# Kernel optimization log

Measured on AMD Instinct MI355X. Metric: run time of the kernel, lower is better.

Reference implementation:

```python
import jax, jax.numpy as jnp
import numpy as np

N_NODES = 100000
N_EDGES = 800000
IN_DIM = 128
NUM_HEADS = 8
HEAD_DIM = 16  # out_dim // num_heads = 128 // 8


def setup_inputs() -> dict:
    key = jax.random.key(0)
    ks = jax.random.split(key, 10)
    scale = 1.0 / np.sqrt(IN_DIM)
    return {
        "x": jax.random.normal(ks[0], (N_NODES, IN_DIM), dtype=jnp.float32),
        "edge_index": jax.random.randint(ks[1], (2, N_EDGES), 0, N_NODES, dtype=jnp.int64),
        "virt_h": jax.random.normal(ks[2], (1, IN_DIM), dtype=jnp.float32),
        "virt_edge_index": jax.random.randint(ks[3], (2, 1), 0, 1, dtype=jnp.int64),
        "Wq": jax.random.normal(ks[4], (IN_DIM, NUM_HEADS * HEAD_DIM), dtype=jnp.float32) * scale,
        "bq": jnp.zeros((NUM_HEADS * HEAD_DIM,), dtype=jnp.float32),
        "Wk": jax.random.normal(ks[5], (IN_DIM, NUM_HEADS * HEAD_DIM), dtype=jnp.float32) * scale,
        "bk": jnp.zeros((NUM_HEADS * HEAD_DIM,), dtype=jnp.float32),
        "Wv": jax.random.normal(ks[6], (IN_DIM, NUM_HEADS * HEAD_DIM), dtype=jnp.float32) * scale,
        "bv": jnp.zeros((NUM_HEADS * HEAD_DIM,), dtype=jnp.float32),
    }


def reference(x, edge_index, virt_h, virt_edge_index, Wq, bq, Wk, bk, Wv, bv):
    # use_virt_nodes=False: virt_h / virt_edge_index are unused dummies.
    n = x.shape[0]
    H, D = NUM_HEADS, HEAD_DIM
    Q = (x @ Wq + bq).reshape(n, H, D)
    K = (x @ Wk + bk).reshape(n, H, D)
    V = (x @ Wv + bv).reshape(n, H, D)

    src = edge_index[0]
    dst = edge_index[1]

    # edge-wise gather QK dot -> clamp -> exp; score: [E, H, 1]
    dot = jnp.sum(K[src] * Q[dst], axis=-1, keepdims=True) / np.sqrt(D).astype(np.float32)
    score = jnp.exp(jnp.clip(dot, -5.0, 5.0))

    msg = V[src] * score  # [E, H, D]
    wV = jax.ops.segment_sum(msg, dst, num_segments=n)     # [N, H, D]
    Z = jax.ops.segment_sum(score, dst, num_segments=n)    # [N, H, 1]

    h_out = (wV / (Z + 1e-6)).reshape(n, H * D)
    return h_out
```

## Files before the change

### kernel.cpp

```cpp
#include <hip/hip_runtime.h>

#define IN_DIM   128
#define NH       8
#define HD       16
#define OUTD     128
#define QKVD     384
#define SH       7
#define NSORTB   64

typedef unsigned short ushort_t;
typedef unsigned int   uint_t;
typedef __bf16 bf16x8 __attribute__((ext_vector_type(8)));
typedef float  f32x4  __attribute__((ext_vector_type(4)));

__device__ __forceinline__ float bf2f(ushort_t u) {
    return __uint_as_float(((uint_t)u) << 16);
}
__device__ __forceinline__ ushort_t f2bf(float f) {
    uint_t u = __float_as_uint(f);
    u += 0x7FFFu + ((u >> 16) & 1u);
    return (ushort_t)(u >> 16);
}

__global__ __launch_bounds__(256) void prep_w(
    const float* __restrict__ Wq, const float* __restrict__ Wk,
    const float* __restrict__ Wv, ushort_t* __restrict__ Wt)
{
    __shared__ float ld[32][33];
    int mat  = blockIdx.x >> 4;
    int tile = blockIdx.x & 15;
    int k0 = (tile >> 2) * 32, c0 = (tile & 3) * 32;
    const float* W = (mat == 0) ? Wq : (mat == 1) ? Wk : Wv;
    int t = threadIdx.x;
    {
        int k = t >> 3, c4 = (t & 7) * 4;
        float4 f = *(const float4*)&W[(size_t)(k0 + k) * 128 + c0 + c4];
        ld[k][c4 + 0] = f.x; ld[k][c4 + 1] = f.y;
        ld[k][c4 + 2] = f.z; ld[k][c4 + 3] = f.w;
    }
    __syncthreads();
    {
        int c = t >> 3, kg = (t & 7) * 4;
        union { ushort_t h[4]; uint2 u; } o;
        o.h[0] = f2bf(ld[kg + 0][c]); o.h[1] = f2bf(ld[kg + 1][c]);
        o.h[2] = f2bf(ld[kg + 2][c]); o.h[3] = f2bf(ld[kg + 3][c]);
        *(uint2*)&Wt[((size_t)(mat * 128 + c0 + c)) * 128 + k0 + kg] = o.u;
    }
}

__global__ __launch_bounds__(384, 3) void fat_gemm_sort(
    const float* __restrict__ x, const ushort_t* __restrict__ Wt,
    const float* __restrict__ bq, const float* __restrict__ bk,
    const float* __restrict__ bv, ushort_t* __restrict__ qkv,
    const int* __restrict__ ei, int* __restrict__ aux,
    uint_t* __restrict__ regions,
    int N, int E, int ntiles, int NBC, int CH)
{
    __shared__ __align__(16) char smem[58448];

    if (blockIdx.x < NSORTB) {
        uint_t* recs = (uint_t*)smem;
        int* hist    = (int*)(smem + 50000);
        int* scn     = (int*)(smem + 54096);
        const int tid = threadIdx.x;
        const int blk = blockIdx.x;
        const int e0g = blk * CH;
        const int e1g = min(E, e0g + CH);
        const int m   = e1g - e0g;

        for (int i = tid; i < 1024; i += 384) hist[i] = 0;
        __syncthreads();
        for (int e = e0g + tid; e < e1g; e += 384)
            atomicAdd(&hist[ei[E + e] >> SH], 1);
        __syncthreads();
        if (tid < 64) {
            int base16 = tid * 16;
            int loc[16]; int s = 0;
#pragma unroll
            for (int i = 0; i < 16; i++) { loc[i] = s; s += hist[base16 + i]; }
            int incl = s;
            for (int off = 1; off < 64; off <<= 1) {
                int t = __shfl_up(incl, off);
                if (tid >= off) incl += t;
            }
            int cexcl = incl - s;
#pragma unroll
            for (int i = 0; i < 16; i++) scn[base16 + i] = cexcl + loc[i];
        }
        __syncthreads();
        for (int b = tid; b < NBC; b += 384) aux[b * NSORTB + blk] = scn[b];
        if (tid == 0) aux[NBC * NSORTB + blk] = m;
        __syncthreads();
        for (int e = e0g + tid; e < e1g; e += 384) {
            int d = ei[E + e];
            int src = ei[e];
            int slot = atomicAdd(&scn[d >> SH], 1);
            recs[slot] = (uint_t)src | ((uint_t)(d & 127) << 20);
        }
        __syncthreads();
        for (int s = tid; s < m; s += 384)
            regions[(size_t)blk * CH + s] = recs[s];
        return;
    }

    ushort_t* sh = (ushort_t*)smem;

    const int tid  = threadIdx.x;
    const int w    = tid >> 6;
    const int quad = (tid >> 4) & 3;
    const int l15  = tid & 15;
    const int colg = w << 6;

    bf16x8 bfr[4][4];
#pragma unroll
    for (int kt = 0; kt < 4; kt++)
#pragma unroll
        for (int cs = 0; cs < 4; cs++) {
            int col = colg + cs * 16 + l15;
            bfr[kt][cs] = *(const bf16x8*)&Wt[(size_t)col * 128 + kt * 32 + quad * 8];
        }

    const int mat = w >> 1;
    const float* Bp = (mat == 0) ? bq : (mat == 1) ? bk : bv;
    float bias[4];
#pragma unroll
    for (int cs = 0; cs < 4; cs++)
        bias[cs] = Bp[((w & 1) << 6) + cs * 16 + l15];

    const int gstride = (int)gridDim.x - NSORTB;
    for (int tile = (int)blockIdx.x - NSORTB; tile < ntiles; tile += gstride) {
        const int row0 = tile * 64;
        __syncthreads();

        for (int ch = tid; ch < 1024; ch += 384) {
            int row = ch >> 4;
            int kc  = ch & 15;
            int grow = row0 + row; if (grow > N - 1) grow = N - 1;
            const float* xp = x + (size_t)grow * IN_DIM + kc * 8;
            float4 f0 = *(const float4*)xp;
            float4 f1 = *(const float4*)(xp + 4);
            union { ushort_t h[8]; uint4 u; } tt;
            tt.h[0] = f2bf(f0.x); tt.h[1] = f2bf(f0.y);
            tt.h[2] = f2bf(f0.z); tt.h[3] = f2bf(f0.w);
            tt.h[4] = f2bf(f1.x); tt.h[5] = f2bf(f1.y);
            tt.h[6] = f2bf(f1.z); tt.h[7] = f2bf(f1.w);
            *(uint4*)&sh[(kc * 65 + row) * 8] = tt.u;
        }
        __syncthreads();

        f32x4 acc[4][4];
#pragma unroll
        for (int r = 0; r < 4; r++)
#pragma unroll
            for (int cs = 0; cs < 4; cs++) acc[r][cs] = (f32x4){0.f, 0.f, 0.f, 0.f};

#pragma unroll
        for (int kt = 0; kt < 4; kt++) {
            int kc = kt * 4 + quad;
            bf16x8 af[4];
#pragma unroll
            for (int r = 0; r < 4; r++)
                af[r] = *(const bf16x8*)&sh[(kc * 65 + r * 16 + l15) * 8];
#pragma unroll
            for (int r = 0; r < 4; r++)
#pragma unroll
                for (int cs = 0; cs < 4; cs++)
                    acc[r][cs] = __builtin_amdgcn_mfma_f32_16x16x32_bf16(
                        af[r], bfr[kt][cs], acc[r][cs], 0, 0, 0);
        }

#define EPS 392
#pragma unroll
        for (int qq = 0; qq < 4; qq++) {
            __syncthreads();
            int lrow = quad << 2;
#pragma unroll
            for (int cs = 0; cs < 4; cs++) {
                int col = (w << 6) + cs * 16 + l15;
#pragma unroll
                for (int reg = 0; reg < 4; reg++)
                    sh[(lrow + reg) * EPS + col] = f2bf(acc[qq][cs][reg] + bias[cs]);
            }
            __syncthreads();
#pragma unroll
            for (int i = 0; i < 2; i++) {
                int c = tid + i * 384;
                int row = c / 48;
                int col = (c % 48) * 8;
                int grow = row0 + qq * 16 + row;
                if (grow < N) {
                    uint4 val = *(const uint4*)&sh[row * EPS + col];
                    *(uint4*)&qkv[(size_t)grow * QKVD + col] = val;
                }
            }
        }
#undef EPS
    }
}

__global__ __launch_bounds__(256) void efine(
    const uint_t* __restrict__ regions, const int* __restrict__ aux,
    int* __restrict__ P, int* __restrict__ sorted_src,
    int N, int NBC, int CH)
{
    __shared__ int rl[64], ro[64], doff[64];
    __shared__ int cnt[128], scn2[128];
    __shared__ uint_t stage[4096];
    __shared__ int    sst[4096];
    __shared__ int s_base;
    const int tid = threadIdx.x;
    const int b   = blockIdx.x;

    if (tid < 64) {
        int r0 = aux[b * NSORTB + tid];
        int r1 = aux[(b + 1) * NSORTB + tid];
        ro[tid] = r0;
        rl[tid] = r1 - r0;
        doff[tid] = r1 - r0;
        int bsum = r0;
#pragma unroll
        for (int off = 1; off < 64; off <<= 1)
            bsum += __shfl_xor(bsum, off);
        if (tid == 0) s_base = bsum;
    }
    __syncthreads();
    for (int off = 1; off < 64; off <<= 1) {
        int v = (tid >= off && tid < 64) ? doff[tid - off] : 0;
        __syncthreads();
        if (tid < 64) doff[tid] += v;
        __syncthreads();
    }
    const int m = doff[63];
    const int base = s_base;

    {
        int r = tid >> 2, k = tid & 3;
        int dst0 = doff[r] - rl[r];
        int src0 = ro[r];
        int len  = rl[r];
        for (int i = k; i < len; i += 4)
            stage[dst0 + i] = regions[(size_t)r * CH + src0 + i];
    }
    __syncthreads();

    if (tid < 128) cnt[tid] = 0;
    __syncthreads();
    for (int i = tid; i < m; i += 256)
        atomicAdd(&cnt[stage[i] >> 20], 1);
    __syncthreads();
    if (tid < 128) scn2[tid] = cnt[tid];
    __syncthreads();
    for (int off = 1; off < 128; off <<= 1) {
        int v = (tid >= off && tid < 128) ? scn2[tid - off] : 0;
        __syncthreads();
        if (tid < 128) scn2[tid] += v;
        __syncthreads();
    }
    if (tid < 128) {
        int excl = scn2[tid] - cnt[tid];
        int n = b * 128 + tid;
        if (n < N) P[n] = base + excl;
        cnt[tid] = excl;
    }
    __syncthreads();
    for (int i = tid; i < m; i += 256) {
        uint_t r = stage[i];
        int pos = atomicAdd(&cnt[r >> 20], 1);
        sst[pos] = (int)(r & 0xFFFFFu);
    }
    __syncthreads();
    for (int i = tid; i < m; i += 256)
        sorted_src[base + i] = sst[i];
}

__global__ __launch_bounds__(256) void segment_attn(
    const ushort_t* __restrict__ qkv,
    const int* __restrict__ P, const int* __restrict__ sorted_src,
    float* __restrict__ out, int N, int E)
{
    int n = (blockIdx.x * 256 + threadIdx.x) >> 4;
    int g = threadIdx.x & 15;
    if (n >= N) return;
    int start = P[n];
    int end   = (n + 1 < N) ? P[n + 1] : E;
    int deg   = end - start;

    const uint_t* qrow = (const uint_t*)(qkv + (size_t)n * QKVD);
    uint4 qu = *(const uint4*)(qrow + g * 4);
    float q0 = bf2f((ushort_t)(qu.x & 0xFFFF)), q1 = bf2f((ushort_t)(qu.x >> 16));
    float q2 = bf2f((ushort_t)(qu.y & 0xFFFF)), q3 = bf2f((ushort_t)(qu.y >> 16));
    float q4 = bf2f((ushort_t)(qu.z & 0xFFFF)), q5 = bf2f((ushort_t)(qu.z >> 16));
    float q6 = bf2f((ushort_t)(qu.w & 0xFFFF)), q7 = bf2f((ushort_t)(qu.w >> 16));

    float a0 = 0.f, a1 = 0.f, a2 = 0.f, a3 = 0.f;
    float a4 = 0.f, a5 = 0.f, a6 = 0.f, a7 = 0.f, z = 0.f;

    int myidx = (g < deg) ? sorted_src[start + g] : 0;
    int wbase = (threadIdx.x & 63) & 48;

#define PROC(ku, vu)                                                       \
    {                                                                      \
        float p = bf2f((ushort_t)((ku).x & 0xFFFF)) * q0                   \
                + bf2f((ushort_t)((ku).x >> 16))    * q1                   \
                + bf2f((ushort_t)((ku).y & 0xFFFF)) * q2                   \
                + bf2f((ushort_t)((ku).y >> 16))    * q3                   \
                + bf2f((ushort_t)((ku).z & 0xFFFF)) * q4                   \
                + bf2f((ushort_t)((ku).z >> 16))    * q5                   \
                + bf2f((ushort_t)((ku).w & 0xFFFF)) * q6                   \
                + bf2f((ushort_t)((ku).w >> 16))    * q7;                  \
        p += __shfl_xor(p, 1);                                             \
        p = fminf(fmaxf(p * 0.25f, -5.f), 5.f);                            \
        float s = __expf(p);                                               \
        a0 += bf2f((ushort_t)((vu).x & 0xFFFF)) * s;                       \
        a1 += bf2f((ushort_t)((vu).x >> 16))    * s;                       \
        a2 += bf2f((ushort_t)((vu).y & 0xFFFF)) * s;                       \
        a3 += bf2f((ushort_t)((vu).y >> 16))    * s;                       \
        a4 += bf2f((ushort_t)((vu).z & 0xFFFF)) * s;                       \
        a5 += bf2f((ushort_t)((vu).z >> 16))    * s;                       \
        a6 += bf2f((ushort_t)((vu).w & 0xFFFF)) * s;                       \
        a7 += bf2f((ushort_t)((vu).w >> 16))    * s;                       \
        z += s;                                                            \
    }

    int cnt = (deg < 16) ? deg : 16;
    int t = 0;
    for (; t + 4 <= cnt; t += 4) {
        int s0 = __shfl(myidx, wbase + t);
        int s1 = __shfl(myidx, wbase + t + 1);
        int s2 = __shfl(myidx, wbase + t + 2);
        int s3 = __shfl(myidx, wbase + t + 3);
        const uint_t* kv0 = (const uint_t*)(qkv + (size_t)s0 * QKVD + 128);
        const uint_t* kv1 = (const uint_t*)(qkv + (size_t)s1 * QKVD + 128);
        const uint_t* kv2 = (const uint_t*)(qkv + (size_t)s2 * QKVD + 128);
        const uint_t* kv3 = (const uint_t*)(qkv + (size_t)s3 * QKVD + 128);
        uint4 ku0 = *(const uint4*)(kv0 + g * 4);
        uint4 ku1 = *(const uint4*)(kv1 + g * 4);
        uint4 ku2 = *(const uint4*)(kv2 + g * 4);
        uint4 ku3 = *(const uint4*)(kv3 + g * 4);
        uint4 vu0 = *(const uint4*)(kv0 + 64 + g * 4);
        uint4 vu1 = *(const uint4*)(kv1 + 64 + g * 4);
        uint4 vu2 = *(const uint4*)(kv2 + 64 + g * 4);
        uint4 vu3 = *(const uint4*)(kv3 + 64 + g * 4);
        PROC(ku0, vu0); PROC(ku1, vu1); PROC(ku2, vu2); PROC(ku3, vu3);
    }
    for (; t + 2 <= cnt; t += 2) {
        int s0 = __shfl(myidx, wbase + t);
        int s1 = __shfl(myidx, wbase + t + 1);
        const uint_t* kv0 = (const uint_t*)(qkv + (size_t)s0 * QKVD + 128);
        const uint_t* kv1 = (const uint_t*)(qkv + (size_t)s1 * QKVD + 128);
        uint4 ku0 = *(const uint4*)(kv0 + g * 4);
        uint4 ku1 = *(const uint4*)(kv1 + g * 4);
        uint4 vu0 = *(const uint4*)(kv0 + 64 + g * 4);
        uint4 vu1 = *(const uint4*)(kv1 + 64 + g * 4);
        PROC(ku0, vu0); PROC(ku1, vu1);
    }
    if (t < cnt) {
        int s0 = __shfl(myidx, wbase + t);
        const uint_t* kv0 = (const uint_t*)(qkv + (size_t)s0 * QKVD + 128);
        uint4 ku0 = *(const uint4*)(kv0 + g * 4);
        uint4 vu0 = *(const uint4*)(kv0 + 64 + g * 4);
        PROC(ku0, vu0);
    }
    for (int j = start + 16; j + 2 <= end; j += 2) {
        int s0 = sorted_src[j];
        int s1 = sorted_src[j + 1];
        const uint_t* kv0 = (const uint_t*)(qkv + (size_t)s0 * QKVD + 128);
        const uint_t* kv1 = (const uint_t*)(qkv + (size_t)s1 * QKVD + 128);
        uint4 ku0 = *(const uint4*)(kv0 + g * 4);
        uint4 ku1 = *(const uint4*)(kv1 + g * 4);
        uint4 vu0 = *(const uint4*)(kv0 + 64 + g * 4);
        uint4 vu1 = *(const uint4*)(kv1 + 64 + g * 4);
        PROC(ku0, vu0); PROC(ku1, vu1);
    }
    if (deg > 16 && ((deg - 16) & 1)) {
        int s0 = sorted_src[end - 1];
        const uint_t* kv0 = (const uint_t*)(qkv + (size_t)s0 * QKVD + 128);
        uint4 ku0 = *(const uint4*)(kv0 + g * 4);
        uint4 vu0 = *(const uint4*)(kv0 + 64 + g * 4);
        PROC(ku0, vu0);
    }
#undef PROC

    float inv = 1.f / (z + 1e-6f);
    f32x4 o0 = {a0 * inv, a1 * inv, a2 * inv, a3 * inv};
    f32x4 o1 = {a4 * inv, a5 * inv, a6 * inv, a7 * inv};
    float* ob = out + (size_t)n * OUTD + g * 8;
    __builtin_nontemporal_store(o0, (f32x4*)ob);
    __builtin_nontemporal_store(o1, (f32x4*)(ob + 4));
}

extern "C" void kernel_launch(void* const* d_in, const int* in_sizes, int n_in,
                              void* d_out, int out_size, void* d_ws, size_t ws_size,
                              hipStream_t stream) {
    const float* x  = (const float*)d_in[0];
    const int*   ei = (const int*)d_in[1];
    const float* Wq = (const float*)d_in[4];
    const float* bq = (const float*)d_in[5];
    const float* Wk = (const float*)d_in[6];
    const float* bk = (const float*)d_in[7];
    const float* Wv = (const float*)d_in[8];
    const float* bv = (const float*)d_in[9];
    float* out = (float*)d_out;

    const int N = in_sizes[0] / IN_DIM;
    const int E = in_sizes[1] / 2;
    const int NBC = (N + 127) >> 7;
    const int CH  = (E + NSORTB - 1) / NSORTB;

    char* wsb = (char*)d_ws;
    ushort_t* qkv = (ushort_t*)wsb;
    ushort_t* Wt  = qkv + (size_t)N * QKVD;
    int* aux = (int*)(Wt + 384 * 128);
    uint_t* regions = (uint_t*)(aux + (NBC + 1) * NSORTB);
    int* sorted = (int*)(regions + (size_t)NSORTB * CH);
    int* P = sorted + E;

    const int ntiles = (N + 63) / 64;

    prep_w<<<48, 256, 0, stream>>>(Wq, Wk, Wv, Wt);
    fat_gemm_sort<<<512, 384, 0, stream>>>(
        x, Wt, bq, bk, bv, qkv, ei, aux, regions, N, E, ntiles, NBC, CH);
    efine<<<NBC, 256, 0, stream>>>(regions, aux, P, sorted, N, NBC, CH);
    segment_attn<<<((size_t)N * 16 + 255) / 256, 256, 0, stream>>>(
        qkv, P, sorted, out, N, E);
}
```

Before: 243.5 us.

## Fuse weight prep, GEMM, sort and attention into one persistent megakernel

```diff
diff --git a/kernel.cpp b/kernel.cpp
--- a/kernel.cpp
+++ b/kernel.cpp
@@ -7,11 +7,14 @@
 #define QKVD     384
 #define SH       7
 #define NSORTB   64
+#define GRID     512
 
 typedef unsigned short ushort_t;
 typedef unsigned int   uint_t;
 typedef __bf16 bf16x8 __attribute__((ext_vector_type(8)));
 typedef float  f32x4  __attribute__((ext_vector_type(4)));
+
+#define AGT __HIP_MEMORY_SCOPE_AGENT
 
 __device__ __forceinline__ float bf2f(ushort_t u) {
     return __uint_as_float(((uint_t)u) << 16);
@@ -21,48 +24,30 @@
     u += 0x7FFFu + ((u >> 16) & 1u);
     return (ushort_t)(u >> 16);
 }
-
-__global__ __launch_bounds__(256) void prep_w(
-    const float* __restrict__ Wq, const float* __restrict__ Wk,
-    const float* __restrict__ Wv, ushort_t* __restrict__ Wt)
-{
-    __shared__ float ld[32][33];
-    int mat  = blockIdx.x >> 4;
-    int tile = blockIdx.x & 15;
-    int k0 = (tile >> 2) * 32, c0 = (tile & 3) * 32;
-    const float* W = (mat == 0) ? Wq : (mat == 1) ? Wk : Wv;
-    int t = threadIdx.x;
-    {
-        int k = t >> 3, c4 = (t & 7) * 4;
-        float4 f = *(const float4*)&W[(size_t)(k0 + k) * 128 + c0 + c4];
-        ld[k][c4 + 0] = f.x; ld[k][c4 + 1] = f.y;
-        ld[k][c4 + 2] = f.z; ld[k][c4 + 3] = f.w;
-    }
-    __syncthreads();
-    {
-        int c = t >> 3, kg = (t & 7) * 4;
-        union { ushort_t h[4]; uint2 u; } o;
-        o.h[0] = f2bf(ld[kg + 0][c]); o.h[1] = f2bf(ld[kg + 1][c]);
-        o.h[2] = f2bf(ld[kg + 2][c]); o.h[3] = f2bf(ld[kg + 3][c]);
-        *(uint2*)&Wt[((size_t)(mat * 128 + c0 + c)) * 128 + k0 + kg] = o.u;
-    }
+__device__ __forceinline__ void wait_ge(int* p, int target) {
+    while (__hip_atomic_load(p, __ATOMIC_RELAXED, AGT) < target)
+        __builtin_amdgcn_s_sleep(8);
 }
 
-__global__ __launch_bounds__(384, 3) void fat_gemm_sort(
-    const float* __restrict__ x, const ushort_t* __restrict__ Wt,
-    const float* __restrict__ bq, const float* __restrict__ bk,
-    const float* __restrict__ bv, ushort_t* __restrict__ qkv,
-    const int* __restrict__ ei, int* __restrict__ aux,
-    uint_t* __restrict__ regions,
-    int N, int E, int ntiles, int NBC, int CH)
+__global__ __launch_bounds__(384, 3) void mega(
+    const float* __restrict__ x,
+    const float* __restrict__ Wq, const float* __restrict__ bq,
+    const float* __restrict__ Wk, const float* __restrict__ bk,
+    const float* __restrict__ Wv, const float* __restrict__ bv,
+    const int* __restrict__ ei,
+    ushort_t* __restrict__ qkv, int* __restrict__ aux,
+    uint_t* __restrict__ regions, int* __restrict__ P,
+    int* __restrict__ sorted_src, float* __restrict__ out,
+    int* ctr, int N, int E, int ntiles, int NBC, int CH)
 {
     __shared__ __align__(16) char smem[58448];
+    __shared__ int s_word;
+    const int tid = threadIdx.x;
 
     if (blockIdx.x < NSORTB) {
         uint_t* recs = (uint_t*)smem;
         int* hist    = (int*)(smem + 50000);
         int* scn     = (int*)(smem + 54096);
-        const int tid = threadIdx.x;
         const int blk = blockIdx.x;
         const int e0g = blk * CH;
         const int e1g = min(E, e0g + CH);
@@ -100,37 +85,138 @@
         __syncthreads();
         for (int s = tid; s < m; s += 384)
             regions[(size_t)blk * CH + s] = recs[s];
-        return;
+        __syncthreads();
+        if (tid == 0)
+            __hip_atomic_fetch_add(&ctr[0], 1, __ATOMIC_RELEASE, AGT);
+    }
+
+    uint_t* stage = (uint_t*)smem;
+    int* sst   = (int*)(smem + 16384);
+    int* rl    = (int*)(smem + 32768);
+    int* ro    = (int*)(smem + 33024);
+    int* doff  = (int*)(smem + 33280);
+    int* cnt   = (int*)(smem + 33536);
+    int* scn2  = (int*)(smem + 34048);
+    int* sbase = (int*)(smem + 34560);
+
+#define EFINE_DRAIN()                                                        \
+    {                                                                        \
+        int cbuckets = 0;                                                    \
+        for (;;) {                                                           \
+            __syncthreads();                                                 \
+            if (tid == 0)                                                    \
+                s_word = __hip_atomic_fetch_add(&ctr[3], 1,                  \
+                                                __ATOMIC_RELAXED, AGT);      \
+            __syncthreads();                                                 \
+            int b = s_word;                                                  \
+            if (b >= NBC) break;                                             \
+            cbuckets++;                                                      \
+            if (tid < 64) {                                                  \
+                int r0 = aux[b * NSORTB + tid];                              \
+                int r1 = aux[(b + 1) * NSORTB + tid];                        \
+                ro[tid] = r0; rl[tid] = r1 - r0; doff[tid] = r1 - r0;        \
+                int bsum = r0;                                               \
+                for (int off = 1; off < 64; off <<= 1)                       \
+                    bsum += __shfl_xor(bsum, off);                           \
+                if (tid == 0) *sbase = bsum;                                 \
+            }                                                                \
+            __syncthreads();                                                 \
+            for (int off = 1; off < 64; off <<= 1) {                         \
+                int v = (tid >= off && tid < 64) ? doff[tid - off] : 0;      \
+                __syncthreads();                                             \
+                if (tid < 64) doff[tid] += v;                                \
+                __syncthreads();                                             \
+            }                                                                \
+            const int m2 = doff[63];                                         \
+            const int base = *sbase;                                         \
+            {                                                                \
+                int r = tid >> 2, k = tid & 3;                               \
+                if (r < 64) {                                                \
+                    int dst0 = doff[r] - rl[r];                              \
+                    int src0 = ro[r];                                        \
+                    int len  = rl[r];                                        \
+                    for (int i = k; i < len; i += 4)                         \
+                        stage[dst0 + i] = regions[(size_t)r * CH + src0 + i];\
+                }                                                            \
+            }                                                                \
+            __syncthreads();                                                 \
+            if (tid < 128) cnt[tid] = 0;                                     \
+            __syncthreads();                                                 \
+            for (int i = tid; i < m2; i += 384)                              \
+                atomicAdd(&cnt[stage[i] >> 20], 1);                          \
+            __syncthreads();                                                 \
+            if (tid < 128) scn2[tid] = cnt[tid];                             \
+            __syncthreads();                                                 \
+            for (int off = 1; off < 128; off <<= 1) {                        \
+                int v = (tid >= off && tid < 128) ? scn2[tid - off] : 0;     \
+                __syncthreads();                                             \
+                if (tid < 128) scn2[tid] += v;                               \
+                __syncthreads();                                             \
+            }                                                                \
+            if (tid < 128) {                                                 \
+                int excl = scn2[tid] - cnt[tid];                             \
+                int n = b * 128 + tid;                                       \
+                if (n < N) P[n] = base + excl;                               \
+                cnt[tid] = excl;                                             \
+            }                                                                \
+            __syncthreads();                                                 \
+            for (int i = tid; i < m2; i += 384) {                            \
+                uint_t rr = stage[i];                                        \
+                int pos = atomicAdd(&cnt[rr >> 20], 1);                      \
+                sst[pos] = (int)(rr & 0xFFFFFu);                             \
+            }                                                                \
+            __syncthreads();                                                 \
+            for (int i = tid; i < m2; i += 384)                              \
+                sorted_src[base + i] = sst[i];                               \
+        }                                                                    \
+        __syncthreads();                                                     \
+        if (tid == 0 && cbuckets)                                            \
+            __hip_atomic_fetch_add(&ctr[4], cbuckets, __ATOMIC_RELEASE, AGT);\
+    }
+
+    if (blockIdx.x < NSORTB) {
+        if (tid == 0) wait_ge(&ctr[0], NSORTB);
+        __syncthreads();
+        (void)__hip_atomic_load(&ctr[0], __ATOMIC_ACQUIRE, AGT);
+        EFINE_DRAIN();
     }
 
     ushort_t* sh = (ushort_t*)smem;
 
-    const int tid  = threadIdx.x;
     const int w    = tid >> 6;
     const int quad = (tid >> 4) & 3;
     const int l15  = tid & 15;
-    const int colg = w << 6;
+    const int mat  = w >> 1;
+    const float* Wsel = (mat == 0) ? Wq : (mat == 1) ? Wk : Wv;
+    const float* Bp   = (mat == 0) ? bq : (mat == 1) ? bk : bv;
 
     bf16x8 bfr[4][4];
 #pragma unroll
     for (int kt = 0; kt < 4; kt++)
 #pragma unroll
         for (int cs = 0; cs < 4; cs++) {
-            int col = colg + cs * 16 + l15;
-            bfr[kt][cs] = *(const bf16x8*)&Wt[(size_t)col * 128 + kt * 32 + quad * 8];
-        }
-
-    const int mat = w >> 1;
-    const float* Bp = (mat == 0) ? bq : (mat == 1) ? bk : bv;
+            int c = ((w & 1) << 6) + cs * 16 + l15;
+            union { ushort_t h[8]; bf16x8 v; } u;
+#pragma unroll
+            for (int j = 0; j < 8; j++)
+                u.h[j] = f2bf(Wsel[(size_t)(kt * 32 + quad * 8 + j) * 128 + c]);
+            bfr[kt][cs] = u.v;
+        }
     float bias[4];
 #pragma unroll
     for (int cs = 0; cs < 4; cs++)
         bias[cs] = Bp[((w & 1) << 6) + cs * 16 + l15];
 
-    const int gstride = (int)gridDim.x - NSORTB;
-    for (int tile = (int)blockIdx.x - NSORTB; tile < ntiles; tile += gstride) {
+    int ctiles = 0;
+    for (;;) {
+        __syncthreads();
+        if (tid == 0)
+            s_word = __hip_atomic_fetch_add(&ctr[1], 1, __ATOMIC_RELAXED, AGT);
+        __syncthreads();
+        const int tile = s_word;
+        if (tile >= ntiles) break;
+        ctiles++;
         const int row0 = tile * 64;
-        __syncthreads();
 
         for (int ch = tid; ch < 1024; ch += 384) {
             int row = ch >> 4;
@@ -196,107 +282,44 @@
         }
 #undef EPS
     }
-}
-
-__global__ __launch_bounds__(256) void efine(
-    const uint_t* __restrict__ regions, const int* __restrict__ aux,
-    int* __restrict__ P, int* __restrict__ sorted_src,
-    int N, int NBC, int CH)
-{
-    __shared__ int rl[64], ro[64], doff[64];
-    __shared__ int cnt[128], scn2[128];
-    __shared__ uint_t stage[4096];
-    __shared__ int    sst[4096];
-    __shared__ int s_base;
-    const int tid = threadIdx.x;
-    const int b   = blockIdx.x;
-
-    if (tid < 64) {
-        int r0 = aux[b * NSORTB + tid];
-        int r1 = aux[(b + 1) * NSORTB + tid];
-        ro[tid] = r0;
-        rl[tid] = r1 - r0;
-        doff[tid] = r1 - r0;
-        int bsum = r0;
-#pragma unroll
-        for (int off = 1; off < 64; off <<= 1)
-            bsum += __shfl_xor(bsum, off);
-        if (tid == 0) s_base = bsum;
-    }
     __syncthreads();
-    for (int off = 1; off < 64; off <<= 1) {
-        int v = (tid >= off && tid < 64) ? doff[tid - off] : 0;
-        __syncthreads();
-        if (tid < 64) doff[tid] += v;
-        __syncthreads();
-    }
-    const int m = doff[63];
-    const int base = s_base;
-
-    {
-        int r = tid >> 2, k = tid & 3;
-        int dst0 = doff[r] - rl[r];
-        int src0 = ro[r];
-        int len  = rl[r];
-        for (int i = k; i < len; i += 4)
-            stage[dst0 + i] = regions[(size_t)r * CH + src0 + i];
+    if (tid == 0 && ctiles)
+        __hip_atomic_fetch_add(&ctr[2], ctiles, __ATOMIC_RELEASE, AGT);
+
+    if (blockIdx.x >= NSORTB) {
+        if (tid == 0) wait_ge(&ctr[0], NSORTB);
+        __syncthreads();
+        (void)__hip_atomic_load(&ctr[0], __ATOMIC_ACQUIRE, AGT);
+        EFINE_DRAIN();
+    }
+#undef EFINE_DRAIN
+
+    if (tid == 0) {
+        wait_ge(&ctr[2], ntiles);
+        wait_ge(&ctr[4], NBC);
     }
     __syncthreads();
-
-    if (tid < 128) cnt[tid] = 0;
-    __syncthreads();
-    for (int i = tid; i < m; i += 256)
-        atomicAdd(&cnt[stage[i] >> 20], 1);
-    __syncthreads();
-    if (tid < 128) scn2[tid] = cnt[tid];
-    __syncthreads();
-    for (int off = 1; off < 128; off <<= 1) {
-        int v = (tid >= off && tid < 128) ? scn2[tid - off] : 0;
-        __syncthreads();
-        if (tid < 128) scn2[tid] += v;
-        __syncthreads();
-    }
-    if (tid < 128) {
-        int excl = scn2[tid] - cnt[tid];
-        int n = b * 128 + tid;
-        if (n < N) P[n] = base + excl;
-        cnt[tid] = excl;
-    }
-    __syncthreads();
-    for (int i = tid; i < m; i += 256) {
-        uint_t r = stage[i];
-        int pos = atomicAdd(&cnt[r >> 20], 1);
-        sst[pos] = (int)(r & 0xFFFFFu);
-    }
-    __syncthreads();
-    for (int i = tid; i < m; i += 256)
-        sorted_src[base + i] = sst[i];
-}
-
-__global__ __launch_bounds__(256) void segment_attn(
-    const ushort_t* __restrict__ qkv,
-    const int* __restrict__ P, const int* __restrict__ sorted_src,
-    float* __restrict__ out, int N, int E)
-{
-    int n = (blockIdx.x * 256 + threadIdx.x) >> 4;
-    int g = threadIdx.x & 15;
-    if (n >= N) return;
-    int start = P[n];
-    int end   = (n + 1 < N) ? P[n + 1] : E;
-    int deg   = end - start;
-
-    const uint_t* qrow = (const uint_t*)(qkv + (size_t)n * QKVD);
-    uint4 qu = *(const uint4*)(qrow + g * 4);
-    float q0 = bf2f((ushort_t)(qu.x & 0xFFFF)), q1 = bf2f((ushort_t)(qu.x >> 16));
-    float q2 = bf2f((ushort_t)(qu.y & 0xFFFF)), q3 = bf2f((ushort_t)(qu.y >> 16));
-    float q4 = bf2f((ushort_t)(qu.z & 0xFFFF)), q5 = bf2f((ushort_t)(qu.z >> 16));
-    float q6 = bf2f((ushort_t)(qu.w & 0xFFFF)), q7 = bf2f((ushort_t)(qu.w >> 16));
-
-    float a0 = 0.f, a1 = 0.f, a2 = 0.f, a3 = 0.f;
-    float a4 = 0.f, a5 = 0.f, a6 = 0.f, a7 = 0.f, z = 0.f;
-
-    int myidx = (g < deg) ? sorted_src[start + g] : 0;
-    int wbase = (threadIdx.x & 63) & 48;
+    (void)__hip_atomic_load(&ctr[2], __ATOMIC_ACQUIRE, AGT);
+    (void)__hip_atomic_load(&ctr[4], __ATOMIC_ACQUIRE, AGT);
+
+    const int g = tid & 15;
+    const int wbase = (tid & 63) & 48;
+    for (int n = blockIdx.x * 24 + (tid >> 4); n < N; n += (int)gridDim.x * 24) {
+        int start = P[n];
+        int end   = (n + 1 < N) ? P[n + 1] : E;
+        int deg   = end - start;
+
+        const uint_t* qrow = (const uint_t*)(qkv + (size_t)n * QKVD);
+        uint4 qu = *(const uint4*)(qrow + g * 4);
+        float q0 = bf2f((ushort_t)(qu.x & 0xFFFF)), q1 = bf2f((ushort_t)(qu.x >> 16));
+        float q2 = bf2f((ushort_t)(qu.y & 0xFFFF)), q3 = bf2f((ushort_t)(qu.y >> 16));
+        float q4 = bf2f((ushort_t)(qu.z & 0xFFFF)), q5 = bf2f((ushort_t)(qu.z >> 16));
+        float q6 = bf2f((ushort_t)(qu.w & 0xFFFF)), q7 = bf2f((ushort_t)(qu.w >> 16));
+
+        float a0 = 0.f, a1 = 0.f, a2 = 0.f, a3 = 0.f;
+        float a4 = 0.f, a5 = 0.f, a6 = 0.f, a7 = 0.f, z = 0.f;
+
+        int myidx = (g < deg) ? sorted_src[start + g] : 0;
 
 #define PROC(ku, vu)                                                       \
     {                                                                      \
@@ -322,71 +345,72 @@
         z += s;                                                            \
     }
 
-    int cnt = (deg < 16) ? deg : 16;
-    int t = 0;
-    for (; t + 4 <= cnt; t += 4) {
-        int s0 = __shfl(myidx, wbase + t);
-        int s1 = __shfl(myidx, wbase + t + 1);
-        int s2 = __shfl(myidx, wbase + t + 2);
-        int s3 = __shfl(myidx, wbase + t + 3);
-        const uint_t* kv0 = (const uint_t*)(qkv + (size_t)s0 * QKVD + 128);
-        const uint_t* kv1 = (const uint_t*)(qkv + (size_t)s1 * QKVD + 128);
-        const uint_t* kv2 = (const uint_t*)(qkv + (size_t)s2 * QKVD + 128);
-        const uint_t* kv3 = (const uint_t*)(qkv + (size_t)s3 * QKVD + 128);
-        uint4 ku0 = *(const uint4*)(kv0 + g * 4);
-        uint4 ku1 = *(const uint4*)(kv1 + g * 4);
-        uint4 ku2 = *(const uint4*)(kv2 + g * 4);
-        uint4 ku3 = *(const uint4*)(kv3 + g * 4);
-        uint4 vu0 = *(const uint4*)(kv0 + 64 + g * 4);
-        uint4 vu1 = *(const uint4*)(kv1 + 64 + g * 4);
-        uint4 vu2 = *(const uint4*)(kv2 + 64 + g * 4);
-        uint4 vu3 = *(const uint4*)(kv3 + 64 + g * 4);
-        PROC(ku0, vu0); PROC(ku1, vu1); PROC(ku2, vu2); PROC(ku3, vu3);
-    }
-    for (; t + 2 <= cnt; t += 2) {
-        int s0 = __shfl(myidx, wbase + t);
-        int s1 = __shfl(myidx, wbase + t + 1);
-        const uint_t* kv0 = (const uint_t*)(qkv + (size_t)s0 * QKVD + 128);
-        const uint_t* kv1 = (const uint_t*)(qkv + (size_t)s1 * QKVD + 128);
-        uint4 ku0 = *(const uint4*)(kv0 + g * 4);
-        uint4 ku1 = *(const uint4*)(kv1 + g * 4);
-        uint4 vu0 = *(const uint4*)(kv0 + 64 + g * 4);
-        uint4 vu1 = *(const uint4*)(kv1 + 64 + g * 4);
-        PROC(ku0, vu0); PROC(ku1, vu1);
-    }
-    if (t < cnt) {
-        int s0 = __shfl(myidx, wbase + t);
-        const uint_t* kv0 = (const uint_t*)(qkv + (size_t)s0 * QKVD + 128);
-        uint4 ku0 = *(const uint4*)(kv0 + g * 4);
-        uint4 vu0 = *(const uint4*)(kv0 + 64 + g * 4);
-        PROC(ku0, vu0);
-    }
-    for (int j = start + 16; j + 2 <= end; j += 2) {
-        int s0 = sorted_src[j];
-        int s1 = sorted_src[j + 1];
-        const uint_t* kv0 = (const uint_t*)(qkv + (size_t)s0 * QKVD + 128);
-        const uint_t* kv1 = (const uint_t*)(qkv + (size_t)s1 * QKVD + 128);
-        uint4 ku0 = *(const uint4*)(kv0 + g * 4);
-        uint4 ku1 = *(const uint4*)(kv1 + g * 4);
-        uint4 vu0 = *(const uint4*)(kv0 + 64 + g * 4);
-        uint4 vu1 = *(const uint4*)(kv1 + 64 + g * 4);
-        PROC(ku0, vu0); PROC(ku1, vu1);
-    }
-    if (deg > 16 && ((deg - 16) & 1)) {
-        int s0 = sorted_src[end - 1];
-        const uint_t* kv0 = (const uint_t*)(qkv + (size_t)s0 * QKVD + 128);
-        uint4 ku0 = *(const uint4*)(kv0 + g * 4);
-        uint4 vu0 = *(const uint4*)(kv0 + 64 + g * 4);
-        PROC(ku0, vu0);
-    }
+        int cnt2 = (deg < 16) ? deg : 16;
+        int t = 0;
+        for (; t + 4 <= cnt2; t += 4) {
+            int s0 = __shfl(myidx, wbase + t);
+            int s1 = __shfl(myidx, wbase + t + 1);
+            int s2 = __shfl(myidx, wbase + t + 2);
+            int s3 = __shfl(myidx, wbase + t + 3);
+            const uint_t* kv0 = (const uint_t*)(qkv + (size_t)s0 * QKVD + 128);
+            const uint_t* kv1 = (const uint_t*)(qkv + (size_t)s1 * QKVD + 128);
+            const uint_t* kv2 = (const uint_t*)(qkv + (size_t)s2 * QKVD + 128);
+            const uint_t* kv3 = (const uint_t*)(qkv + (size_t)s3 * QKVD + 128);
+            uint4 ku0 = *(const uint4*)(kv0 + g * 4);
+            uint4 ku1 = *(const uint4*)(kv1 + g * 4);
+            uint4 ku2 = *(const uint4*)(kv2 + g * 4);
+            uint4 ku3 = *(const uint4*)(kv3 + g * 4);
+            uint4 vu0 = *(const uint4*)(kv0 + 64 + g * 4);
+            uint4 vu1 = *(const uint4*)(kv1 + 64 + g * 4);
+            uint4 vu2 = *(const uint4*)(kv2 + 64 + g * 4);
+            uint4 vu3 = *(const uint4*)(kv3 + 64 + g * 4);
+            PROC(ku0, vu0); PROC(ku1, vu1); PROC(ku2, vu2); PROC(ku3, vu3);
+        }
+        for (; t + 2 <= cnt2; t += 2) {
+            int s0 = __shfl(myidx, wbase + t);
+            int s1 = __shfl(myidx, wbase + t + 1);
+            const uint_t* kv0 = (const uint_t*)(qkv + (size_t)s0 * QKVD + 128);
+            const uint_t* kv1 = (const uint_t*)(qkv + (size_t)s1 * QKVD + 128);
+            uint4 ku0 = *(const uint4*)(kv0 + g * 4);
+            uint4 ku1 = *(const uint4*)(kv1 + g * 4);
+            uint4 vu0 = *(const uint4*)(kv0 + 64 + g * 4);
+            uint4 vu1 = *(const uint4*)(kv1 + 64 + g * 4);
+            PROC(ku0, vu0); PROC(ku1, vu1);
+        }
+        if (t < cnt2) {
+            int s0 = __shfl(myidx, wbase + t);
+            const uint_t* kv0 = (const uint_t*)(qkv + (size_t)s0 * QKVD + 128);
+            uint4 ku0 = *(const uint4*)(kv0 + g * 4);
+            uint4 vu0 = *(const uint4*)(kv0 + 64 + g * 4);
+            PROC(ku0, vu0);
+        }
+        for (int j = start + 16; j + 2 <= end; j += 2) {
+            int s0 = sorted_src[j];
+            int s1 = sorted_src[j + 1];
+            const uint_t* kv0 = (const uint_t*)(qkv + (size_t)s0 * QKVD + 128);
+            const uint_t* kv1 = (const uint_t*)(qkv + (size_t)s1 * QKVD + 128);
+            uint4 ku0 = *(const uint4*)(kv0 + g * 4);
+            uint4 ku1 = *(const uint4*)(kv1 + g * 4);
+            uint4 vu0 = *(const uint4*)(kv0 + 64 + g * 4);
+            uint4 vu1 = *(const uint4*)(kv1 + 64 + g * 4);
+            PROC(ku0, vu0); PROC(ku1, vu1);
+        }
+        if (deg > 16 && ((deg - 16) & 1)) {
+            int s0 = sorted_src[end - 1];
+            const uint_t* kv0 = (const uint_t*)(qkv + (size_t)s0 * QKVD + 128);
+            uint4 ku0 = *(const uint4*)(kv0 + g * 4);
+            uint4 vu0 = *(const uint4*)(kv0 + 64 + g * 4);
+            PROC(ku0, vu0);
+        }
 #undef PROC
 
-    float inv = 1.f / (z + 1e-6f);
-    f32x4 o0 = {a0 * inv, a1 * inv, a2 * inv, a3 * inv};
-    f32x4 o1 = {a4 * inv, a5 * inv, a6 * inv, a7 * inv};
-    float* ob = out + (size_t)n * OUTD + g * 8;
-    __builtin_nontemporal_store(o0, (f32x4*)ob);
-    __builtin_nontemporal_store(o1, (f32x4*)(ob + 4));
+        float inv = 1.f / (z + 1e-6f);
+        f32x4 o0 = {a0 * inv, a1 * inv, a2 * inv, a3 * inv};
+        f32x4 o1 = {a4 * inv, a5 * inv, a6 * inv, a7 * inv};
+        float* ob = out + (size_t)n * OUTD + g * 8;
+        __builtin_nontemporal_store(o0, (f32x4*)ob);
+        __builtin_nontemporal_store(o1, (f32x4*)(ob + 4));
+    }
 }
 
 extern "C" void kernel_launch(void* const* d_in, const int* in_sizes, int n_in,
@@ -406,21 +430,19 @@
     const int E = in_sizes[1] / 2;
     const int NBC = (N + 127) >> 7;
     const int CH  = (E + NSORTB - 1) / NSORTB;
+    const int ntiles = (N + 63) / 64;
 
     char* wsb = (char*)d_ws;
     ushort_t* qkv = (ushort_t*)wsb;
-    ushort_t* Wt  = qkv + (size_t)N * QKVD;
-    int* aux = (int*)(Wt + 384 * 128);
+    int* aux = (int*)(qkv + (size_t)N * QKVD);
     uint_t* regions = (uint_t*)(aux + (NBC + 1) * NSORTB);
     int* sorted = (int*)(regions + (size_t)NSORTB * CH);
     int* P = sorted + E;
-
-    const int ntiles = (N + 63) / 64;
-
-    prep_w<<<48, 256, 0, stream>>>(Wq, Wk, Wv, Wt);
-    fat_gemm_sort<<<512, 384, 0, stream>>>(
-        x, Wt, bq, bk, bv, qkv, ei, aux, regions, N, E, ntiles, NBC, CH);
-    efine<<<NBC, 256, 0, stream>>>(regions, aux, P, sorted, N, NBC, CH);
-    segment_attn<<<((size_t)N * 16 + 255) / 256, 256, 0, stream>>>(
-        qkv, P, sorted, out, N, E);
+    int* ctr = P + N;
+
+    hipMemsetAsync(ctr, 0, 32, stream);
+    mega<<<GRID, 384, 0, stream>>>(
+        x, Wq, bq, Wk, bk, Wv, bv, ei,
+        qkv, aux, regions, P, sorted, out, ctr,
+        N, E, ntiles, NBC, CH);
 }
```

Result: slower. 415.4 us (+70.6%).
